# Kernel optimization log

Measured on AMD Instinct MI355X. Metric: run time of the kernel, lower is better.

Reference implementation:

```python
import jax, jax.numpy as jnp
import numpy as np

B, N, E, H, SD, HID = 4, 512, 1024, 16, 64, 64
D = E // H  # head_dim


def setup_inputs() -> dict:
    key = jax.random.key(0)
    ks = jax.random.split(key, 20)
    s = lambda i, shape, scale: (jax.random.normal(ks[i], shape, dtype=jnp.float32) * scale)
    inp = {
        "query": s(0, (B, N, E), 1.0),
        "key": s(1, (B, N, E), 1.0),
        "value": s(2, (B, N, E), 1.0),
        "state_embeddings": s(3, (B, N, SD), 1.0),
        # projection weights stored [in, out] (transposed vs torch nn.Linear)
        "Wq": s(4, (E, E), E ** -0.5), "bq": jnp.zeros((E,), jnp.float32),
        "Wk": s(5, (E, E), E ** -0.5), "bk": jnp.zeros((E,), jnp.float32),
        "Wv": s(6, (E, E), E ** -0.5), "bv": jnp.zeros((E,), jnp.float32),
        "Wo": s(7, (E, E), E ** -0.5), "bo": jnp.zeros((E,), jnp.float32),
        # CAB compatibility MLP: Linear(2*SD->HID), ReLU, Linear(HID->HID), ReLU, Linear(HID->H)
        "W1": s(8, (2 * SD, HID), (2 * SD) ** -0.5), "b1": jnp.zeros((HID,), jnp.float32),
        "W2": s(9, (HID, HID), HID ** -0.5), "b2": jnp.zeros((HID,), jnp.float32),
        "W3": s(10, (HID, H), HID ** -0.5), "b3": jnp.zeros((H,), jnp.float32),
        "head_temps": jnp.ones((H,), jnp.float32),
    }
    return inp


def reference(query, key, value, state_embeddings,
              Wq, bq, Wk, bk, Wv, bv, Wo, bo,
              W1, b1, W2, b2, W3, b3, head_temps):
    scale = D ** -0.5
    q = (query @ Wq + bq).reshape(B, N, H, D)
    k = (key @ Wk + bk).reshape(B, N, H, D)
    v = (value @ Wv + bv).reshape(B, N, H, D)
    # [B, H, T, S]
    scores = jnp.einsum("bthd,bshd->bhts", q, k) * scale

    # CAB bias: MLP([e_i; e_j]) -> split first layer to avoid materializing pairs
    hi = state_embeddings @ W1[:SD]          # [B, N, HID]
    hj = state_embeddings @ W1[SD:]          # [B, N, HID]
    h = jax.nn.relu(hi[:, :, None, :] + hj[:, None, :, :] + b1)  # [B, N, N, HID]
    h = jax.nn.relu(h @ W2 + b2)
    comp = h @ W3 + b3                        # [B, N, N, H]
    bias = jnp.transpose(comp, (0, 3, 1, 2)) * head_temps[None, :, None, None]
    scores = scores + bias

    attn = jax.nn.softmax(scores, axis=-1)
    out = jnp.einsum("bhts,bshd->bthd", attn, v).reshape(B, N, E)
    return out @ Wo + bo
```

## Files before the change

### kernel.cpp

```cpp
#include <hip/hip_runtime.h>
#include <hip/hip_bf16.h>

typedef unsigned short u16;
typedef short short8 __attribute__((ext_vector_type(8)));
typedef float f32x4 __attribute__((ext_vector_type(4)));
typedef unsigned short u16x4 __attribute__((ext_vector_type(4)));

#define BB 4
#define NS 512
#define EE 1024
#define HH 16
#define DD 64
#define MM (BB*NS)
#define NSQ 2
#define SQW (NS/NSQ)

__device__ __forceinline__ u16 f2bfh(float x) {
  __hip_bfloat16 h = __float2bfloat16(x);
  union { __hip_bfloat16 h; u16 u; } c; c.h = h; return c.u;
}
__device__ __forceinline__ unsigned pkbf(float a, float b) {
  union { __hip_bfloat16 h; u16 u; } ca, cb;
  ca.h = __float2bfloat16(a); cb.h = __float2bfloat16(b);
  return (unsigned)ca.u | ((unsigned)cb.u << 16);
}
union S8 { short8 s; unsigned u[4]; };

__device__ __forceinline__ void gload_lds16(const void* g, void* l) {
  __builtin_amdgcn_global_load_lds(
      (const __attribute__((address_space(1))) unsigned int*)g,
      (__attribute__((address_space(3))) unsigned int*)l, 16, 0, 0);
}


__global__ void cvt_w(const float* __restrict__ Wq, const float* __restrict__ Wk,
                      const float* __restrict__ Wv, const float* __restrict__ Wo,
                      const float* __restrict__ W2, const float* __restrict__ W3,
                      const float* __restrict__ q, const float* __restrict__ k,
                      const float* __restrict__ v,
                      const float* __restrict__ se, const float* __restrict__ W1,
                      const float* __restrict__ b1,
                      u16* __restrict__ WqT, u16* __restrict__ WkT,
                      u16* __restrict__ WvT, u16* __restrict__ WoT,
                      u16* __restrict__ W2T, u16* __restrict__ W3P,
                      u16* __restrict__ qb, u16* __restrict__ kb, u16* __restrict__ vb,
                      float* __restrict__ hi, float* __restrict__ hj) {
  int z = blockIdx.z;
  if (z == 8) {
    int flat = blockIdx.y * 32 + blockIdx.x;
    if (flat >= 512) return;
    int tid = threadIdx.x;
    int row = flat * 4 + (tid >> 6);
    int c = tid & 63;
    float ah = b1[c], aj = 0.f;
    #pragma unroll 8
    for (int kk = 0; kk < 64; ++kk) {
      float s = se[row * 64 + kk];
      ah += s * W1[kk * 64 + c];
      aj += s * W1[(kk + 64) * 64 + c];
    }
    hi[row * 64 + c] = ah;
    hj[row * 64 + c] = aj;
    return;
  }
  if (z >= 5) {
    int seg = z - 5;
    const float* src = seg == 0 ? q : (seg == 1 ? k : v);
    u16* dst = seg == 0 ? qb : (seg == 1 ? kb : vb);
    size_t flat = ((size_t)blockIdx.y * 32 + blockIdx.x) * 256 + threadIdx.x;
    size_t off = flat << 3;
    float4 f0 = *(const float4*)(src + off);
    float4 f1 = *(const float4*)(src + off + 4);
    S8 r;
    r.u[0] = pkbf(f0.x, f0.y); r.u[1] = pkbf(f0.z, f0.w);
    r.u[2] = pkbf(f1.x, f1.y); r.u[3] = pkbf(f1.z, f1.w);
    *(short8*)(dst + off) = r.s;
    return;
  }
  if (z == 4) {
    if (blockIdx.x || blockIdx.y) return;
    int tid = threadIdx.x;
    for (int i = tid; i < 4096; i += 256) {
      int n = i >> 6, kk = i & 63;
      W2T[i] = f2bfh(W2[kk * 64 + n]);
    }
    for (int i = tid; i < 1024; i += 256) {
      int h = i >> 6, rem = i & 63;
      int k2 = rem >> 5, gg = (rem >> 3) & 3, j = rem & 7;
      int c = (2 * k2 + (j >> 2)) * 16 + gg * 4 + (j & 3);
      W3P[i] = f2bfh(W3[c * 16 + h]);
    }
    return;
  }
  const float* W = z == 0 ? Wq : z == 1 ? Wk : z == 2 ? Wv : Wo;
  u16* WT = z == 0 ? WqT : z == 1 ? WkT : z == 2 ? WvT : WoT;
  int n0 = blockIdx.x << 5, k0 = blockIdx.y << 5;
  __shared__ float tile[32][33];
  int tx = threadIdx.x & 31, ty = threadIdx.x >> 5;
  #pragma unroll
  for (int i = 0; i < 4; ++i) {
    int r = (i << 3) + ty;
    tile[r][tx] = W[(size_t)(k0 + r) * EE + n0 + tx];
  }
  __syncthreads();
  #pragma unroll
  for (int i = 0; i < 4; ++i) {
    int r = (i << 3) + ty;
    WT[(size_t)(n0 + r) * EE + k0 + tx] = f2bfh(tile[tx][r]);
  }
}


template <int MODE>
__device__ __forceinline__ void gemm_body(const u16* __restrict__ A, const u16* __restrict__ Bt,
                                          const float* __restrict__ bias, void* __restrict__ Cout) {
  __shared__ u16 As[128 * 32];
  __shared__ u16 Bs[128 * 32];
  const int tid = threadIdx.x, lane = tid & 63, wave = tid >> 6;
  const int m0 = blockIdx.x * 128, n0 = blockIdx.y * 128;
  const int wr = wave >> 1, wc = wave & 1;

  const f32x4 zero = {0.f, 0.f, 0.f, 0.f};
  f32x4 acc[4][4];
  #pragma unroll
  for (int i = 0; i < 4; ++i)
    #pragma unroll
    for (int j = 0; j < 4; ++j) acc[i][j] = zero;

  const int rA = lane >> 2;
  const int cA = (lane & 3) << 3;

  for (int kt = 0; kt < EE; kt += 32) {
    #pragma unroll
    for (int i = 0; i < 2; ++i) {
      int base = ((i << 2) + wave) << 9;
      int row = (base >> 5) + rA;
      gload_lds16(A  + (size_t)(m0 + row) * EE + kt + cA, As + base);
      gload_lds16(Bt + (size_t)(n0 + row) * EE + kt + cA, Bs + base);
    }
    __syncthreads();
    short8 af[4], bfr[4];
    #pragma unroll
    for (int mf = 0; mf < 4; ++mf) {
      int row = wr * 64 + mf * 16 + (lane & 15);
      af[mf] = *(const short8*)(As + row * 32 + ((lane >> 4) << 3));
    }
    #pragma unroll
    for (int nf = 0; nf < 4; ++nf) {
      int row = wc * 64 + nf * 16 + (lane & 15);
      bfr[nf] = *(const short8*)(Bs + row * 32 + ((lane >> 4) << 3));
    }
    #pragma unroll
    for (int mf = 0; mf < 4; ++mf)
      #pragma unroll
      for (int nf = 0; nf < 4; ++nf)
        acc[mf][nf] = __builtin_amdgcn_mfma_f32_16x16x32_bf16(af[mf], bfr[nf], acc[mf][nf], 0, 0, 0);
    __syncthreads();
  }

  #pragma unroll
  for (int mf = 0; mf < 4; ++mf) {
    #pragma unroll
    for (int nf = 0; nf < 4; ++nf) {
      int col = n0 + wc * 64 + nf * 16 + (lane & 15);
      float bv = bias[col];
      #pragma unroll
      for (int j = 0; j < 4; ++j) {
        int rowm = m0 + wr * 64 + mf * 16 + ((lane >> 4) << 2) + j;
        float v = acc[mf][nf][j] + bv;
        int bb = rowm >> 9, r = rowm & 511;
        int h = col >> 6, d = col & 63;
        size_t off;
        if (MODE == 0)
          off = ((((size_t)bb * HH + h) * 32 + (r >> 4)) << 10) + ((size_t)(d >> 5) << 9)
              + ((size_t)((((d >> 3) & 3) << 4) + (r & 15)) << 3) + (d & 7);
        else
          off = (((((size_t)bb * HH + h) * 16 + (r >> 5)) * 4 + (d >> 4)) << 9)
              + ((size_t)((((r >> 3) & 3) << 4) + (d & 15)) << 3) + (r & 7);
        ((u16*)Cout)[off] = f2bfh(v);
      }
    }
  }
}

__global__ __launch_bounds__(256, 2) void gemm_proj(
    const u16* __restrict__ qb, const u16* __restrict__ kb, const u16* __restrict__ vb,
    const u16* __restrict__ WqT, const u16* __restrict__ WkT, const u16* __restrict__ WvT,
    const float* __restrict__ bq, const float* __restrict__ bk, const float* __restrict__ bv_,
    u16* __restrict__ qF, u16* __restrict__ kF, u16* __restrict__ vF) {
  int z = blockIdx.z;
  if (z == 0)      gemm_body<0>(qb, WqT, bq, qF);
  else if (z == 1) gemm_body<0>(kb, WkT, bk, kF);
  else             gemm_body<1>(vb, WvT, bv_, vF);
}


__global__ __launch_bounds__(256, 2) void gemm_final64(
    const u16* __restrict__ A, const u16* __restrict__ Bt,
    const float* __restrict__ bias, float* __restrict__ C) {
  __shared__ u16 As[64 * 32];
  __shared__ u16 Bs[128 * 32];
  const int tid = threadIdx.x, lane = tid & 63, wave = tid >> 6;
  const int m0 = blockIdx.x * 64, n0 = blockIdx.y * 128;
  const int wr = wave >> 1, wc = wave & 1;

  const f32x4 zero = {0.f, 0.f, 0.f, 0.f};
  f32x4 acc[2][4];
  #pragma unroll
  for (int i = 0; i < 2; ++i)
    #pragma unroll
    for (int j = 0; j < 4; ++j) acc[i][j] = zero;

  const int rA = lane >> 2;
  const int cA = (lane & 3) << 3;

  for (int kt = 0; kt < EE; kt += 32) {
    {
      int base = wave << 9;
      int row = (wave << 4) + rA;
      gload_lds16(A + (size_t)(m0 + row) * EE + kt + cA, As + base);
    }
    #pragma unroll
    for (int i = 0; i < 2; ++i) {
      int base = ((i << 2) + wave) << 9;
      int row = (base >> 5) + rA;
      gload_lds16(Bt + (size_t)(n0 + row) * EE + kt + cA, Bs + base);
    }
    __syncthreads();
    short8 af[2], bfr[4];
    #pragma unroll
    for (int mf = 0; mf < 2; ++mf) {
      int row = wr * 32 + mf * 16 + (lane & 15);
      af[mf] = *(const short8*)(As + row * 32 + ((lane >> 4) << 3));
    }
    #pragma unroll
    for (int nf = 0; nf < 4; ++nf) {
      int row = wc * 64 + nf * 16 + (lane & 15);
      bfr[nf] = *(const short8*)(Bs + row * 32 + ((lane >> 4) << 3));
    }
    #pragma unroll
    for (int mf = 0; mf < 2; ++mf)
      #pragma unroll
      for (int nf = 0; nf < 4; ++nf)
        acc[mf][nf] = __builtin_amdgcn_mfma_f32_16x16x32_bf16(af[mf], bfr[nf], acc[mf][nf], 0, 0, 0);
    __syncthreads();
  }

  #pragma unroll
  for (int mf = 0; mf < 2; ++mf)
    #pragma unroll
    for (int nf = 0; nf < 4; ++nf) {
      int col = n0 + wc * 64 + nf * 16 + (lane & 15);
      float bv = bias[col];
      #pragma unroll
      for (int j = 0; j < 4; ++j) {
        int rowm = m0 + wr * 32 + mf * 16 + ((lane >> 4) << 2) + j;
        C[(size_t)rowm * EE + col] = acc[mf][nf][j] + bv;
      }
    }
}


__global__ __launch_bounds__(512, 2) void fused_cab_attn(
    const float* __restrict__ hi, const float* __restrict__ hj,
    const u16* __restrict__ W2T, const u16* __restrict__ W3P,
    const float* __restrict__ b2, const float* __restrict__ b3,
    const float* __restrict__ temps,
    const u16* __restrict__ qF, const u16* __restrict__ kF,
    const u16* __restrict__ vF,
    float* __restrict__ Opart, float* __restrict__ mlpart) {
  const int b = blockIdx.x >> 1, sq = blockIdx.x & 1, tt = blockIdx.y;
  const int t0 = tt << 4;
  const int tid = threadIdx.x, lane = tid & 63, wave = tid >> 6;
  const int g = lane >> 4, sl = lane & 15;

  __shared__ float hi_s[16][80];
  __shared__ float hj_s[2][32][65];
  __shared__ float b2_s[64], b3_s[16], tp_s[16];
  __shared__ float comp3[16 * 273];
  __shared__ u16 Pl[8][16][40];

  if (tid < 256) {
    int r = tid >> 4, c4 = (tid & 15) << 2;
    float4 hv = *(const float4*)(hi + ((size_t)(b * NS + t0 + r) << 6) + c4);
    *(f32x4*)&hi_s[r][c4] = (f32x4){hv.x, hv.y, hv.z, hv.w};
  } else {
    int ix = tid - 256;
    if (ix < 64) b2_s[ix] = b2[ix];
    else if (ix < 80) b3_s[ix - 64] = b3[ix - 64];
    else if (ix < 96) tp_s[ix - 80] = temps[ix - 80];
  }

  const int hr = tid >> 4, hc4 = (tid & 15) << 2;
  {
    float4 a = *(const float4*)(hj + ((size_t)(b * NS + sq * SQW + hr) << 6) + hc4);
    hj_s[0][hr][hc4 + 0] = a.x; hj_s[0][hr][hc4 + 1] = a.y;
    hj_s[0][hr][hc4 + 2] = a.z; hj_s[0][hr][hc4 + 3] = a.w;
  }

  const f32x4 zero = {0.f, 0.f, 0.f, 0.f};
  f32x4 acc[2][4];
  #pragma unroll
  for (int i = 0; i < 2; ++i)
    #pragma unroll
    for (int j = 0; j < 4; ++j) acc[i][j] = zero;
  float m_run[2] = {-3e38f, -3e38f};
  float l_run[2] = {0.f, 0.f};

  int cur = 0;
  for (int pr = 0; pr < 8; ++pr) {
    const int s0p = sq * SQW + (pr << 5);
    __syncthreads();

    float4 hjnx;
    const bool have = (pr + 1) < 8;
    if (have)
      hjnx = *(const float4*)(hj + ((size_t)(b * NS + s0p + 32 + hr) << 6) + hc4);

    float vsc[2][2][4];

    #pragma unroll
    for (int ta = 0; ta < 2; ++ta) {
      if (ta) __syncthreads();
      {
        float hjv[2][8];
        #pragma unroll
        for (int kk = 0; kk < 2; ++kk)
          #pragma unroll
          for (int j = 0; j < 8; ++j)
            hjv[kk][j] = hj_s[cur][(ta << 4) + sl][kk * 32 + (g << 3) + j];

        short8 w3f[2];
        #pragma unroll
        for (int k2 = 0; k2 < 2; ++k2)
          w3f[k2] = *(const short8*)(W3P + (sl << 6) + k2 * 32 + (g << 3));

        float b2v[4][4];
        #pragma unroll
        for (int mfc = 0; mfc < 4; ++mfc)
          #pragma unroll
          for (int jj = 0; jj < 4; ++jj)
            b2v[mfc][jj] = b2_s[mfc * 16 + (g << 2) + jj];

        #pragma unroll
        for (int q = 0; q < 2; ++q) {
          int tl = (wave << 1) + q;
          short8 xb[2];
          #pragma unroll
          for (int kk = 0; kk < 2; ++kk) {
            int c0 = kk * 32 + (g << 3);
            f32x4 h0 = *(const f32x4*)&hi_s[tl][c0];
            f32x4 h1 = *(const f32x4*)&hi_s[tl][c0 + 4];
            float x[8];
            #pragma unroll
            for (int j = 0; j < 4; ++j) {
              x[j]     = fmaxf(h0[j] + hjv[kk][j], 0.f);
              x[j + 4] = fmaxf(h1[j] + hjv[kk][j + 4], 0.f);
            }
            S8 r;
            r.u[0] = pkbf(x[0], x[1]); r.u[1] = pkbf(x[2], x[3]);
            r.u[2] = pkbf(x[4], x[5]); r.u[3] = pkbf(x[6], x[7]);
            xb[kk] = r.s;
          }
          f32x4 accY[4];
          #pragma unroll
          for (int i = 0; i < 4; ++i) accY[i] = zero;
          #pragma unroll
          for (int kk = 0; kk < 2; ++kk)
            #pragma unroll
            for (int mfc = 0; mfc < 4; ++mfc) {
              short8 w2 = *(const short8*)(W2T + ((mfc * 16 + sl) << 6) + kk * 32 + (g << 3));
              accY[mfc] = __builtin_amdgcn_mfma_f32_16x16x32_bf16(w2, xb[kk], accY[mfc], 0, 0, 0);
            }
          f32x4 compD = zero;
          #pragma unroll
          for (int k2 = 0; k2 < 2; ++k2) {
            float y[8];
            #pragma unroll
            for (int j = 0; j < 4; ++j) {
              y[j]     = fmaxf(accY[2 * k2][j]     + b2v[2 * k2][j],     0.f);
              y[j + 4] = fmaxf(accY[2 * k2 + 1][j] + b2v[2 * k2 + 1][j], 0.f);
            }
            S8 r;
            r.u[0] = pkbf(y[0], y[1]); r.u[1] = pkbf(y[2], y[3]);
            r.u[2] = pkbf(y[4], y[5]); r.u[3] = pkbf(y[6], y[7]);
            compD = __builtin_amdgcn_mfma_f32_16x16x32_bf16(w3f[k2], r.s, compD, 0, 0, 0);
          }
          #pragma unroll
          for (int jj = 0; jj < 4; ++jj) {
            int h = (g << 2) + jj;
            comp3[h * 273 + sl * 17 + tl] = (compD[jj] + b3_s[h]) * tp_s[h];
          }
        }
      }
      __syncthreads();
      const int s16 = (sq << 4) + (pr << 1) + ta;
      #pragma unroll
      for (int hh = 0; hh < 2; ++hh) {
        int h = (wave << 1) + hh;
        const u16* qb_ = qF + ((((size_t)b * HH + h) * 32 + tt) << 10) + (lane << 3);
        const u16* kb_ = kF + ((((size_t)b * HH + h) * 32 + s16) << 10) + (lane << 3);
        f32x4 accS = zero;
        accS = __builtin_amdgcn_mfma_f32_16x16x32_bf16(*(const short8*)kb_, *(const short8*)qb_, accS, 0, 0, 0);
        accS = __builtin_amdgcn_mfma_f32_16x16x32_bf16(*(const short8*)(kb_ + 512), *(const short8*)(qb_ + 512), accS, 0, 0, 0);
        #pragma unroll
        for (int j = 0; j < 4; ++j)
          vsc[ta][hh][j] = accS[j] * 0.125f + comp3[h * 273 + ((g << 2) + j) * 17 + sl];
      }
    }

    if (have) {
      hj_s[cur ^ 1][hr][hc4 + 0] = hjnx.x; hj_s[cur ^ 1][hr][hc4 + 1] = hjnx.y;
      hj_s[cur ^ 1][hr][hc4 + 2] = hjnx.z; hj_s[cur ^ 1][hr][hc4 + 3] = hjnx.w;
    }

    #pragma unroll
    for (int hh = 0; hh < 2; ++hh) {
      int h = (wave << 1) + hh;
      float e[8];
      float mx = -3e38f;
      #pragma unroll
      for (int j = 0; j < 4; ++j)
        mx = fmaxf(mx, fmaxf(vsc[0][hh][j], vsc[1][hh][j]));
      mx = fmaxf(mx, __shfl_xor(mx, 16, 64));
      mx = fmaxf(mx, __shfl_xor(mx, 32, 64));
      float mnew = fmaxf(m_run[hh], mx);
      float c = __expf(m_run[hh] - mnew);
      m_run[hh] = mnew;
      #pragma unroll
      for (int ta = 0; ta < 2; ++ta)
        #pragma unroll
        for (int j = 0; j < 4; ++j)
          e[ta * 4 + j] = __expf(vsc[ta][hh][j] - mnew);
      float ps = ((e[0] + e[1]) + (e[2] + e[3])) + ((e[4] + e[5]) + (e[6] + e[7]));
      ps += __shfl_xor(ps, 16, 64);
      ps += __shfl_xor(ps, 32, 64);
      l_run[hh] = l_run[hh] * c + ps;

      uint2 wA; wA.x = pkbf(e[0], e[1]); wA.y = pkbf(e[2], e[3]);
      uint2 wB; wB.x = pkbf(e[4], e[5]); wB.y = pkbf(e[6], e[7]);
      *(uint2*)&Pl[wave][sl][(g << 2)]      = wA;
      *(uint2*)&Pl[wave][sl][16 + (g << 2)] = wB;
      short8 pf = *(const short8*)&Pl[wave][sl][(g << 3)];

      float cb[4];
      #pragma unroll
      for (int j = 0; j < 4; ++j) cb[j] = __shfl(c, (g << 2) + j, 64);

      const u16* vb0 = vF + (((((size_t)b * HH + h) * 16 + (sq << 3) + pr) * 4) << 9) + (lane << 3);
      #pragma unroll
      for (int nf = 0; nf < 4; ++nf) {
        #pragma unroll
        for (int j = 0; j < 4; ++j) acc[hh][nf][j] *= cb[j];
        short8 vv = *(const short8*)(vb0 + ((size_t)nf << 9));
        acc[hh][nf] = __builtin_amdgcn_mfma_f32_16x16x32_bf16(pf, vv, acc[hh][nf], 0, 0, 0);
      }
    }
    cur ^= 1;
  }

  size_t obase = ((size_t)sq * MM + (size_t)b * NS + t0) * EE;
  #pragma unroll
  for (int hh = 0; hh < 2; ++hh) {
    int h = (wave << 1) + hh;
    #pragma unroll
    for (int nf = 0; nf < 4; ++nf)
      #pragma unroll
      for (int j = 0; j < 4; ++j)
        Opart[obase + (size_t)((g << 2) + j) * EE + (h << 6) + nf * 16 + sl] = acc[hh][nf][j];
  }
  if (g == 0) {
    #pragma unroll
    for (int hh = 0; hh < 2; ++hh) {
      int h = (wave << 1) + hh;
      size_t mlb = (((size_t)sq * MM + b * NS + t0 + sl) * HH + h) * 2;
      mlpart[mlb] = m_run[hh];
      mlpart[mlb + 1] = l_run[hh];
    }
  }
}


__global__ void combine_pv(const float* __restrict__ Opart, const float* __restrict__ mlpart,
                           u16* __restrict__ attn_out) {
  int row = blockIdx.x;
  int tid = threadIdx.x;
  int c4 = tid << 2;
  int h = c4 >> 6;
  float m[NSQ], l[NSQ];
  #pragma unroll
  for (int pq = 0; pq < NSQ; ++pq) {
    size_t mb = (((size_t)pq * MM + row) * HH + h) * 2;
    m[pq] = mlpart[mb]; l[pq] = mlpart[mb + 1];
  }
  float M = m[0];
  #pragma unroll
  for (int pq = 1; pq < NSQ; ++pq) M = fmaxf(M, m[pq]);
  float den = 0.f;
  f32x4 num = {0.f, 0.f, 0.f, 0.f};
  #pragma unroll
  for (int pq = 0; pq < NSQ; ++pq) {
    float w = __expf(m[pq] - M);
    den += w * l[pq];
    f32x4 o = *(const f32x4*)(Opart + ((size_t)pq * MM + row) * EE + c4);
    #pragma unroll
    for (int i = 0; i < 4; ++i) num[i] += w * o[i];
  }
  float r = 1.0f / den;
  u16x4 out;
  #pragma unroll
  for (int i = 0; i < 4; ++i) out[i] = f2bfh(num[i] * r);
  *(u16x4*)(attn_out + (size_t)row * EE + c4) = out;
}


extern "C" void kernel_launch(void* const* d_in, const int* in_sizes, int n_in,
                              void* d_out, int out_size, void* d_ws, size_t ws_size,
                              hipStream_t stream) {
  const float* query = (const float*)d_in[0];
  const float* key   = (const float*)d_in[1];
  const float* value = (const float*)d_in[2];
  const float* se    = (const float*)d_in[3];
  const float* Wq = (const float*)d_in[4];  const float* bq = (const float*)d_in[5];
  const float* Wk = (const float*)d_in[6];  const float* bk = (const float*)d_in[7];
  const float* Wv = (const float*)d_in[8];  const float* bv = (const float*)d_in[9];
  const float* Wo = (const float*)d_in[10]; const float* bo = (const float*)d_in[11];
  const float* W1 = (const float*)d_in[12]; const float* b1 = (const float*)d_in[13];
  const float* W2 = (const float*)d_in[14]; const float* b2 = (const float*)d_in[15];
  const float* W3 = (const float*)d_in[16]; const float* b3 = (const float*)d_in[17];
  const float* temps = (const float*)d_in[18];

  char* p = (char*)d_ws;
  auto alloc = [&](size_t bytes) { char* r = p; p += (bytes + 255) & ~(size_t)255; return r; };
  u16* qb  = (u16*)alloc((size_t)MM * EE * 2);
  u16* kb  = (u16*)alloc((size_t)MM * EE * 2);
  u16* vb  = (u16*)alloc((size_t)MM * EE * 2);
  u16* WqT = (u16*)alloc((size_t)EE * EE * 2);
  u16* WkT = (u16*)alloc((size_t)EE * EE * 2);
  u16* WvT = (u16*)alloc((size_t)EE * EE * 2);
  u16* WoT = (u16*)alloc((size_t)EE * EE * 2);
  u16* W2T = (u16*)alloc(4096 * 2);
  u16* W3P = (u16*)alloc(1024 * 2);
  u16* qF  = (u16*)alloc((size_t)MM * EE * 2);
  u16* kF  = (u16*)alloc((size_t)MM * EE * 2);
  u16* vF  = (u16*)alloc((size_t)MM * EE * 2);
  float* hi = (float*)alloc((size_t)MM * 64 * 4);
  float* hj = (float*)alloc((size_t)MM * 64 * 4);
  float* Opart = (float*)alloc((size_t)NSQ * MM * EE * 4);
  float* mlpart = (float*)alloc((size_t)NSQ * MM * HH * 2 * 4);
  u16* attn_out = (u16*)alloc((size_t)MM * EE * 2);
  (void)ws_size; (void)in_sizes; (void)n_in; (void)out_size;

  cvt_w<<<dim3(32, 32, 9), 256, 0, stream>>>(Wq, Wk, Wv, Wo, W2, W3, query, key, value,
                                             se, W1, b1,
                                             WqT, WkT, WvT, WoT, W2T, W3P, qb, kb, vb,
                                             hi, hj);
  gemm_proj<<<dim3(16, 8, 3), 256, 0, stream>>>(qb, kb, vb, WqT, WkT, WvT, bq, bk, bv, qF, kF, vF);
  fused_cab_attn<<<dim3(8, 32, 1), 512, 0, stream>>>(hi, hj, W2T, W3P, b2, b3, temps,
                                                     qF, kF, vF, Opart, mlpart);
  combine_pv<<<MM, 256, 0, stream>>>(Opart, mlpart, attn_out);
  gemm_final64<<<dim3(32, 8), 256, 0, stream>>>(attn_out, WoT, bo, (float*)d_out);
}
```

Measured before the change: 115.5 us.

## Use 16 waves per block, one head and one query row per wave

```diff
diff --git a/kernel.cpp b/kernel.cpp
--- a/kernel.cpp
+++ b/kernel.cpp
@@ -261,7 +261,7 @@
 }
 
 
-__global__ __launch_bounds__(512, 2) void fused_cab_attn(
+__global__ __launch_bounds__(1024, 4) void fused_cab_attn(
     const float* __restrict__ hi, const float* __restrict__ hj,
     const u16* __restrict__ W2T, const u16* __restrict__ W3P,
     const float* __restrict__ b2, const float* __restrict__ b3,
@@ -273,12 +273,13 @@
   const int t0 = tt << 4;
   const int tid = threadIdx.x, lane = tid & 63, wave = tid >> 6;
   const int g = lane >> 4, sl = lane & 15;
+  const int h = wave;
 
   __shared__ float hi_s[16][80];
   __shared__ float hj_s[2][32][65];
   __shared__ float b2_s[64], b3_s[16], tp_s[16];
   __shared__ float comp3[16 * 273];
-  __shared__ u16 Pl[8][16][40];
+  __shared__ u16 Pl[16][16][40];
 
   if (tid < 256) {
     int r = tid >> 4, c4 = (tid & 15) << 2;
@@ -291,33 +292,30 @@
     else if (ix < 96) tp_s[ix - 80] = temps[ix - 80];
   }
 
-  const int hr = tid >> 4, hc4 = (tid & 15) << 2;
+  const int hr = tid >> 5, hc2 = (tid & 31) << 1;
   {
-    float4 a = *(const float4*)(hj + ((size_t)(b * NS + sq * SQW + hr) << 6) + hc4);
-    hj_s[0][hr][hc4 + 0] = a.x; hj_s[0][hr][hc4 + 1] = a.y;
-    hj_s[0][hr][hc4 + 2] = a.z; hj_s[0][hr][hc4 + 3] = a.w;
+    float2 a = *(const float2*)(hj + ((size_t)(b * NS + sq * SQW + hr) << 6) + hc2);
+    hj_s[0][hr][hc2 + 0] = a.x; hj_s[0][hr][hc2 + 1] = a.y;
   }
 
   const f32x4 zero = {0.f, 0.f, 0.f, 0.f};
-  f32x4 acc[2][4];
-  #pragma unroll
-  for (int i = 0; i < 2; ++i)
-    #pragma unroll
-    for (int j = 0; j < 4; ++j) acc[i][j] = zero;
-  float m_run[2] = {-3e38f, -3e38f};
-  float l_run[2] = {0.f, 0.f};
+  f32x4 acc[4];
+  #pragma unroll
+  for (int j = 0; j < 4; ++j) acc[j] = zero;
+  float m_run = -3e38f;
+  float l_run = 0.f;
 
   int cur = 0;
   for (int pr = 0; pr < 8; ++pr) {
     const int s0p = sq * SQW + (pr << 5);
     __syncthreads();
 
-    float4 hjnx;
+    float2 hjnx;
     const bool have = (pr + 1) < 8;
     if (have)
-      hjnx = *(const float4*)(hj + ((size_t)(b * NS + s0p + 32 + hr) << 6) + hc4);
-
-    float vsc[2][2][4];
+      hjnx = *(const float2*)(hj + ((size_t)(b * NS + s0p + 32 + hr) << 6) + hc2);
+
+    float vsc[2][4];
 
     #pragma unroll
     for (int ta = 0; ta < 2; ++ta) {
@@ -342,62 +340,57 @@
           for (int jj = 0; jj < 4; ++jj)
             b2v[mfc][jj] = b2_s[mfc * 16 + (g << 2) + jj];
 
-        #pragma unroll
-        for (int q = 0; q < 2; ++q) {
-          int tl = (wave << 1) + q;
-          short8 xb[2];
+        const int tl = wave;
+        short8 xb[2];
+        #pragma unroll
+        for (int kk = 0; kk < 2; ++kk) {
+          int c0 = kk * 32 + (g << 3);
+          f32x4 h0 = *(const f32x4*)&hi_s[tl][c0];
+          f32x4 h1 = *(const f32x4*)&hi_s[tl][c0 + 4];
+          float x[8];
           #pragma unroll
-          for (int kk = 0; kk < 2; ++kk) {
-            int c0 = kk * 32 + (g << 3);
-            f32x4 h0 = *(const f32x4*)&hi_s[tl][c0];
-            f32x4 h1 = *(const f32x4*)&hi_s[tl][c0 + 4];
-            float x[8];
-            #pragma unroll
-            for (int j = 0; j < 4; ++j) {
-              x[j]     = fmaxf(h0[j] + hjv[kk][j], 0.f);
-              x[j + 4] = fmaxf(h1[j] + hjv[kk][j + 4], 0.f);
-            }
-            S8 r;
-            r.u[0] = pkbf(x[0], x[1]); r.u[1] = pkbf(x[2], x[3]);
-            r.u[2] = pkbf(x[4], x[5]); r.u[3] = pkbf(x[6], x[7]);
-            xb[kk] = r.s;
+          for (int j = 0; j < 4; ++j) {
+            x[j]     = fmaxf(h0[j] + hjv[kk][j], 0.f);
+            x[j + 4] = fmaxf(h1[j] + hjv[kk][j + 4], 0.f);
           }
-          f32x4 accY[4];
+          S8 r;
+          r.u[0] = pkbf(x[0], x[1]); r.u[1] = pkbf(x[2], x[3]);
+          r.u[2] = pkbf(x[4], x[5]); r.u[3] = pkbf(x[6], x[7]);
+          xb[kk] = r.s;
+        }
+        f32x4 accY[4];
+        #pragma unroll
+        for (int i = 0; i < 4; ++i) accY[i] = zero;
+        #pragma unroll
+        for (int kk = 0; kk < 2; ++kk)
           #pragma unroll
-          for (int i = 0; i < 4; ++i) accY[i] = zero;
+          for (int mfc = 0; mfc < 4; ++mfc) {
+            short8 w2 = *(const short8*)(W2T + ((mfc * 16 + sl) << 6) + kk * 32 + (g << 3));
+            accY[mfc] = __builtin_amdgcn_mfma_f32_16x16x32_bf16(w2, xb[kk], accY[mfc], 0, 0, 0);
+          }
+        f32x4 compD = zero;
+        #pragma unroll
+        for (int k2 = 0; k2 < 2; ++k2) {
+          float y[8];
           #pragma unroll
-          for (int kk = 0; kk < 2; ++kk)
-            #pragma unroll
-            for (int mfc = 0; mfc < 4; ++mfc) {
-              short8 w2 = *(const short8*)(W2T + ((mfc * 16 + sl) << 6) + kk * 32 + (g << 3));
-              accY[mfc] = __builtin_amdgcn_mfma_f32_16x16x32_bf16(w2, xb[kk], accY[mfc], 0, 0, 0);
-            }
-          f32x4 compD = zero;
-          #pragma unroll
-          for (int k2 = 0; k2 < 2; ++k2) {
-            float y[8];
-            #pragma unroll
-            for (int j = 0; j < 4; ++j) {
-              y[j]     = fmaxf(accY[2 * k2][j]     + b2v[2 * k2][j],     0.f);
-              y[j + 4] = fmaxf(accY[2 * k2 + 1][j] + b2v[2 * k2 + 1][j], 0.f);
-            }
-            S8 r;
-            r.u[0] = pkbf(y[0], y[1]); r.u[1] = pkbf(y[2], y[3]);
-            r.u[2] = pkbf(y[4], y[5]); r.u[3] = pkbf(y[6], y[7]);
-            compD = __builtin_amdgcn_mfma_f32_16x16x32_bf16(w3f[k2], r.s, compD, 0, 0, 0);
+          for (int j = 0; j < 4; ++j) {
+            y[j]     = fmaxf(accY[2 * k2][j]     + b2v[2 * k2][j],     0.f);
+            y[j + 4] = fmaxf(accY[2 * k2 + 1][j] + b2v[2 * k2 + 1][j], 0.f);
           }
-          #pragma unroll
-          for (int jj = 0; jj < 4; ++jj) {
-            int h = (g << 2) + jj;
-            comp3[h * 273 + sl * 17 + tl] = (compD[jj] + b3_s[h]) * tp_s[h];
-          }
+          S8 r;
+          r.u[0] = pkbf(y[0], y[1]); r.u[1] = pkbf(y[2], y[3]);
+          r.u[2] = pkbf(y[4], y[5]); r.u[3] = pkbf(y[6], y[7]);
+          compD = __builtin_amdgcn_mfma_f32_16x16x32_bf16(w3f[k2], r.s, compD, 0, 0, 0);
+        }
+        #pragma unroll
+        for (int jj = 0; jj < 4; ++jj) {
+          int hw = (g << 2) + jj;
+          comp3[hw * 273 + sl * 17 + tl] = (compD[jj] + b3_s[jj + (g << 2) - (g << 2) + (g << 2)]) * tp_s[(g << 2) + jj];
         }
       }
       __syncthreads();
       const int s16 = (sq << 4) + (pr << 1) + ta;
-      #pragma unroll
-      for (int hh = 0; hh < 2; ++hh) {
-        int h = (wave << 1) + hh;
+      {
         const u16* qb_ = qF + ((((size_t)b * HH + h) * 32 + tt) << 10) + (lane << 3);
         const u16* kb_ = kF + ((((size_t)b * HH + h) * 32 + s16) << 10) + (lane << 3);
         f32x4 accS = zero;
@@ -405,37 +398,35 @@
         accS = __builtin_amdgcn_mfma_f32_16x16x32_bf16(*(const short8*)(kb_ + 512), *(const short8*)(qb_ + 512), accS, 0, 0, 0);
         #pragma unroll
         for (int j = 0; j < 4; ++j)
-          vsc[ta][hh][j] = accS[j] * 0.125f + comp3[h * 273 + ((g << 2) + j) * 17 + sl];
+          vsc[ta][j] = accS[j] * 0.125f + comp3[h * 273 + ((g << 2) + j) * 17 + sl];
       }
     }
 
     if (have) {
-      hj_s[cur ^ 1][hr][hc4 + 0] = hjnx.x; hj_s[cur ^ 1][hr][hc4 + 1] = hjnx.y;
-      hj_s[cur ^ 1][hr][hc4 + 2] = hjnx.z; hj_s[cur ^ 1][hr][hc4 + 3] = hjnx.w;
-    }
-
-    #pragma unroll
-    for (int hh = 0; hh < 2; ++hh) {
-      int h = (wave << 1) + hh;
+      hj_s[cur ^ 1][hr][hc2 + 0] = hjnx.x;
+      hj_s[cur ^ 1][hr][hc2 + 1] = hjnx.y;
+    }
+
+    {
       float e[8];
       float mx = -3e38f;
       #pragma unroll
       for (int j = 0; j < 4; ++j)
-        mx = fmaxf(mx, fmaxf(vsc[0][hh][j], vsc[1][hh][j]));
+        mx = fmaxf(mx, fmaxf(vsc[0][j], vsc[1][j]));
       mx = fmaxf(mx, __shfl_xor(mx, 16, 64));
       mx = fmaxf(mx, __shfl_xor(mx, 32, 64));
-      float mnew = fmaxf(m_run[hh], mx);
-      float c = __expf(m_run[hh] - mnew);
-      m_run[hh] = mnew;
+      float mnew = fmaxf(m_run, mx);
+      float c = __expf(m_run - mnew);
+      m_run = mnew;
       #pragma unroll
       for (int ta = 0; ta < 2; ++ta)
         #pragma unroll
         for (int j = 0; j < 4; ++j)
-          e[ta * 4 + j] = __expf(vsc[ta][hh][j] - mnew);
+          e[ta * 4 + j] = __expf(vsc[ta][j] - mnew);
       float ps = ((e[0] + e[1]) + (e[2] + e[3])) + ((e[4] + e[5]) + (e[6] + e[7]));
       ps += __shfl_xor(ps, 16, 64);
       ps += __shfl_xor(ps, 32, 64);
-      l_run[hh] = l_run[hh] * c + ps;
+      l_run = l_run * c + ps;
 
       uint2 wA; wA.x = pkbf(e[0], e[1]); wA.y = pkbf(e[2], e[3]);
       uint2 wB; wB.x = pkbf(e[4], e[5]); wB.y = pkbf(e[6], e[7]);
@@ -451,9 +442,9 @@
       #pragma unroll
       for (int nf = 0; nf < 4; ++nf) {
         #pragma unroll
-        for (int j = 0; j < 4; ++j) acc[hh][nf][j] *= cb[j];
+        for (int j = 0; j < 4; ++j) acc[nf][j] *= cb[j];
         short8 vv = *(const short8*)(vb0 + ((size_t)nf << 9));
-        acc[hh][nf] = __builtin_amdgcn_mfma_f32_16x16x32_bf16(pf, vv, acc[hh][nf], 0, 0, 0);
+        acc[nf] = __builtin_amdgcn_mfma_f32_16x16x32_bf16(pf, vv, acc[nf], 0, 0, 0);
       }
     }
     cur ^= 1;
@@ -461,22 +452,14 @@
 
   size_t obase = ((size_t)sq * MM + (size_t)b * NS + t0) * EE;
   #pragma unroll
-  for (int hh = 0; hh < 2; ++hh) {
-    int h = (wave << 1) + hh;
-    #pragma unroll
-    for (int nf = 0; nf < 4; ++nf)
-      #pragma unroll
-      for (int j = 0; j < 4; ++j)
-        Opart[obase + (size_t)((g << 2) + j) * EE + (h << 6) + nf * 16 + sl] = acc[hh][nf][j];
-  }
+  for (int nf = 0; nf < 4; ++nf)
+    #pragma unroll
+    for (int j = 0; j < 4; ++j)
+      Opart[obase + (size_t)((g << 2) + j) * EE + (h << 6) + nf * 16 + sl] = acc[nf][j];
   if (g == 0) {
-    #pragma unroll
-    for (int hh = 0; hh < 2; ++hh) {
-      int h = (wave << 1) + hh;
-      size_t mlb = (((size_t)sq * MM + b * NS + t0 + sl) * HH + h) * 2;
-      mlpart[mlb] = m_run[hh];
-      mlpart[mlb + 1] = l_run[hh];
-    }
+    size_t mlb = (((size_t)sq * MM + b * NS + t0 + sl) * HH + h) * 2;
+    mlpart[mlb] = m_run;
+    mlpart[mlb + 1] = l_run;
   }
 }
 
@@ -556,8 +539,8 @@
                                              WqT, WkT, WvT, WoT, W2T, W3P, qb, kb, vb,
                                              hi, hj);
   gemm_proj<<<dim3(16, 8, 3), 256, 0, stream>>>(qb, kb, vb, WqT, WkT, WvT, bq, bk, bv, qF, kF, vF);
-  fused_cab_attn<<<dim3(8, 32, 1), 512, 0, stream>>>(hi, hj, W2T, W3P, b2, b3, temps,
-                                                     qF, kF, vF, Opart, mlpart);
+  fused_cab_attn<<<dim3(8, 32, 1), 1024, 0, stream>>>(hi, hj, W2T, W3P, b2, b3, temps,
+                                                      qF, kF, vF, Opart, mlpart);
   combine_pv<<<MM, 256, 0, stream>>>(Opart, mlpart, attn_out);
   gemm_final64<<<dim3(32, 8), 256, 0, stream>>>(attn_out, WoT, bo, (float*)d_out);
 }
```

New measurement: 132.3 us. +14.5%, slower.
